# Kernel optimization log

Measured on AMD Instinct MI355X. Metric: run time of the kernel, lower is better.

## Reference

```python
import jax, jax.numpy as jnp
import numpy as np

N_NODES = 100000


def _gcn_conv(x, W, b, src, dst, deg_inv_sqrt):
    # linear transform first (PyG GCNConv order): [N, F] @ [F, H]
    h = x @ W
    # symmetric normalization per edge: deg^-1/2[src] * deg^-1/2[dst]
    norm = deg_inv_sqrt[src] * deg_inv_sqrt[dst]
    msg = h[src] * norm[:, None]  # [E, H]
    out = jax.ops.segment_sum(msg, dst, num_segments=N_NODES)
    return out + b


def setup_inputs() -> dict:
    key = jax.random.key(0)
    k1, k2, k3, k4 = jax.random.split(key, 4)
    F_IN, H = 512, 512
    E = 800000
    x = jax.random.normal(k1, (N_NODES, F_IN), dtype=jnp.float32)
    edge_index = jax.random.randint(k2, (2, E), 0, N_NODES, dtype=jnp.int64)
    W1 = jax.random.normal(k3, (F_IN, H), dtype=jnp.float32) * (1.0 / np.sqrt(F_IN))
    b1 = jnp.zeros((H,), dtype=jnp.float32)
    W2 = jax.random.normal(k4, (H, H), dtype=jnp.float32) * (1.0 / np.sqrt(H))
    b2 = jnp.zeros((H,), dtype=jnp.float32)
    return {"x": x, "edge_index": edge_index, "W1": W1, "b1": b1, "W2": W2, "b2": b2}


def reference(x, edge_index, W1, b1, W2, b2):
    # add self loops (PyG GCNConv default add_self_loops=True)
    loop = jnp.arange(N_NODES, dtype=edge_index.dtype)
    src = jnp.concatenate([edge_index[0], loop])
    dst = jnp.concatenate([edge_index[1], loop])
    # degree of destination nodes (including self loops)
    deg = jax.ops.segment_sum(jnp.ones_like(dst, dtype=x.dtype), dst, num_segments=N_NODES)
    deg_inv_sqrt = jnp.where(deg > 0, jax.lax.rsqrt(jnp.maximum(deg, 1.0)), 0.0)
    h = jax.nn.relu(_gcn_conv(x, W1, b1, src, dst, deg_inv_sqrt))
    # dropout is identity at inference (training=False)
    out = _gcn_conv(h, W2, b2, src, dst, deg_inv_sqrt)
    return out
```

## Files before the change

kernel.cpp:

```cpp
#include <hip/hip_runtime.h>

#define N_NODES 100000
#define E_EDGES 800000
#define E_TOT   900000
#define F 512

typedef __attribute__((ext_vector_type(8))) short short8;
typedef __attribute__((ext_vector_type(4))) float f32x4;
typedef unsigned int u32;

__device__ __forceinline__ float bfu(unsigned int u) {
    union { unsigned int i; float f; } c; c.i = u << 16; return c.f;
}
__device__ __forceinline__ unsigned short f2b(float f) {
    union { float f; unsigned int u; } c; c.f = f;
    return (unsigned short)((c.u + 0x7fffu + ((c.u >> 16) & 1u)) >> 16);
}
__device__ __forceinline__ float fbits(unsigned int u) {
    union { unsigned int i; float f; } c; c.i = u; return c.f;
}
__device__ __forceinline__ unsigned int bits(float f) {
    union { float f; unsigned int i; } c; c.f = f; return c.i;
}
__device__ __forceinline__ void gload_lds16(const void* g, void* l) {
    __builtin_amdgcn_global_load_lds(
        (const __attribute__((address_space(1))) u32*)g,
        (__attribute__((address_space(3))) u32*)l, 16, 0, 0);
}

__global__ void k_init(unsigned int* deg, unsigned int* counter) {
    int i = blockIdx.x * 256 + threadIdx.x;
    if (i < N_NODES) deg[i] = 1u;
    if (i == 0) *counter = 0u;
}

__global__ void k_hist(const int* __restrict__ ei, unsigned int* deg) {
    int e = blockIdx.x * 256 + threadIdx.x;
    if (e < E_EDGES) atomicAdd(&deg[ei[E_EDGES + e]], 1u);
}

__global__ void k_disalloc(const unsigned int* __restrict__ deg, unsigned int* counter,
                           float* __restrict__ dis,
                           int2* __restrict__ seg, unsigned int* __restrict__ cursor) {
    int i = blockIdx.x * 256 + threadIdx.x;
    if (i < N_NODES) {
        unsigned int d = deg[i];
        dis[i] = rsqrtf((float)d);
        unsigned int p = atomicAdd(counter, d);
        seg[i] = make_int2((int)p, (int)(p + d));
        cursor[i] = p;
    }
}

__global__ void k_scatter(const int* __restrict__ ei, const float* __restrict__ dis,
                          unsigned int* __restrict__ cursor,
                          uint2* __restrict__ ev) {
    int e = blockIdx.x * 256 + threadIdx.x;
    if (e < E_TOT) {
        int s, d;
        if (e < E_EDGES) { s = ei[e]; d = ei[E_EDGES + e]; }
        else             { s = e - E_EDGES; d = s; }
        unsigned int p = atomicAdd(&cursor[d], 1u);
        ev[p] = make_uint2((unsigned)s, bits(dis[s] * dis[d]));
    }
}

__global__ void k_cvtX(const float* __restrict__ xin, unsigned short* __restrict__ xb) {
    int i = blockIdx.x * 256 + threadIdx.x;
    const f32x4* p = (const f32x4*)xin + (size_t)i * 2;
    f32x4 a = __builtin_nontemporal_load(p);
    f32x4 b = __builtin_nontemporal_load(p + 1);
    uint4 o;
    o.x = (unsigned)f2b(a[0]) | ((unsigned)f2b(a[1]) << 16);
    o.y = (unsigned)f2b(a[2]) | ((unsigned)f2b(a[3]) << 16);
    o.z = (unsigned)f2b(b[0]) | ((unsigned)f2b(b[1]) << 16);
    o.w = (unsigned)f2b(b[2]) | ((unsigned)f2b(b[3]) << 16);
    *(uint4*)(xb + (size_t)i * 8) = o;
}

__global__ void k_cvtW(const float* __restrict__ W1, const float* __restrict__ W2,
                       unsigned short* __restrict__ W1t, unsigned short* __restrict__ W2t) {
    int t = blockIdx.x * 256 + threadIdx.x;
    int which = t >= F * F;
    int u = t - which * F * F;
    int n = u >> 9, k = u & 511;
    const float* W = which ? W2 : W1;
    unsigned short* Wt = which ? W2t : W1t;
    Wt[u] = f2b(W[k * F + n]);
}

__global__ __launch_bounds__(256)
void gemm_bt(const unsigned short* __restrict__ A, const unsigned short* __restrict__ Bt,
             const float* __restrict__ bias,
             unsigned short* __restrict__ outb, float* __restrict__ outf,
             int relu, int M) {
    __shared__ unsigned short lsa[2][128 * 32];
    __shared__ unsigned short lsb[2][128 * 32];
    int bx = blockIdx.x;
    int by = blockIdx.y;
    int t  = threadIdx.x;
    int lane = t & 63, w = t >> 6;
    int wr = w >> 1, wc = w & 1;

    f32x4 acc[4][4];
    #pragma unroll
    for (int m = 0; m < 4; ++m)
        #pragma unroll
        for (int n = 0; n < 4; ++n)
            acc[m][n] = (f32x4){0.f, 0.f, 0.f, 0.f};

    int rowBase = bx * 128;

    int ar[2], br[2], akc[2];
    #pragma unroll
    for (int i = 0; i < 2; ++i) {
        int idx = i * 256 + t;
        int r = idx >> 2;
        akc[i] = (idx & 3) * 8;
        int ga = rowBase + r; if (ga >= M) ga = M - 1;
        ar[i] = ga;
        br[i] = by * 128 + r;
    }

    auto STAGE = [&](int buf, int k0) {
        #pragma unroll
        for (int i = 0; i < 2; ++i) {
            int idx = i * 256 + t;
            gload_lds16(A + (size_t)ar[i] * F + k0 + akc[i], &lsa[buf][idx * 8]);
            gload_lds16(Bt + (size_t)br[i] * F + k0 + akc[i], &lsb[buf][idx * 8]);
        }
    };
    auto COMPUTE = [&](int buf) {
        int koff = (lane >> 4) * 8;
        int rsel = lane & 15;
        short8 af[4], bfr[4];
        #pragma unroll
        for (int m = 0; m < 4; ++m)
            af[m] = *(short8*)&lsa[buf][(wr * 64 + m * 16 + rsel) * 32 + koff];
        #pragma unroll
        for (int n = 0; n < 4; ++n)
            bfr[n] = *(short8*)&lsb[buf][(wc * 64 + n * 16 + rsel) * 32 + koff];
        #pragma unroll
        for (int m = 0; m < 4; ++m)
            #pragma unroll
            for (int n = 0; n < 4; ++n)
                acc[m][n] = __builtin_amdgcn_mfma_f32_16x16x32_bf16(af[m], bfr[n], acc[m][n], 0, 0, 0);
    };

    STAGE(0, 0);
    __syncthreads();
    #pragma unroll
    for (int kp = 0; kp < 8; ++kp) {
        STAGE(1, (2 * kp + 1) * 32);
        COMPUTE(0);
        __syncthreads();
        if (kp < 7) STAGE(0, (2 * kp + 2) * 32);
        COMPUTE(1);
        __syncthreads();
    }

    int rq = (lane >> 4) * 4, cq = lane & 15;
    #pragma unroll
    for (int m = 0; m < 4; ++m)
        #pragma unroll
        for (int n = 0; n < 4; ++n) {
            int colv = by * 128 + wc * 64 + n * 16 + cq;
            float bv = bias[colv];
            #pragma unroll
            for (int j = 0; j < 4; ++j) {
                int row = rowBase + wr * 64 + m * 16 + rq + j;
                if (row < M) {
                    float v = acc[m][n][j] + bv;
                    if (relu) v = fmaxf(v, 0.f);
                    if (outb) outb[(size_t)row * F + colv] = f2b(v);
                    else __builtin_nontemporal_store(v, outf + (size_t)row * F + colv);
                }
            }
        }
}

__global__ __launch_bounds__(256)
void k_agg(const unsigned short* __restrict__ hin, const int2* __restrict__ seg,
           const uint2* __restrict__ ev,
           unsigned short* __restrict__ outb) {
    int node = blockIdx.x * 4 + (threadIdx.x >> 6);
    int lane = threadIdx.x & 63;
    if (node >= N_NODES) return;
    int2 se = seg[node];
    int e0 = se.x, e1 = se.y;
    float acc[8] = {0, 0, 0, 0, 0, 0, 0, 0};
    const unsigned short* base = hin + lane * 8;

    int e = e0;
    for (; e + 3 < e1; e += 4) {
        uint2 p0 = ev[e], p1 = ev[e + 1], p2 = ev[e + 2], p3 = ev[e + 3];
        uint4 v0 = *(const uint4*)(base + ((size_t)p0.x << 9));
        uint4 v1 = *(const uint4*)(base + ((size_t)p1.x << 9));
        uint4 v2 = *(const uint4*)(base + ((size_t)p2.x << 9));
        uint4 v3 = *(const uint4*)(base + ((size_t)p3.x << 9));
        float w0 = fbits(p0.y), w1 = fbits(p1.y), w2 = fbits(p2.y), w3 = fbits(p3.y);
        acc[0] += w0 * bfu(v0.x & 0xffffu); acc[1] += w0 * bfu(v0.x >> 16);
        acc[2] += w0 * bfu(v0.y & 0xffffu); acc[3] += w0 * bfu(v0.y >> 16);
        acc[4] += w0 * bfu(v0.z & 0xffffu); acc[5] += w0 * bfu(v0.z >> 16);
        acc[6] += w0 * bfu(v0.w & 0xffffu); acc[7] += w0 * bfu(v0.w >> 16);
        acc[0] += w1 * bfu(v1.x & 0xffffu); acc[1] += w1 * bfu(v1.x >> 16);
        acc[2] += w1 * bfu(v1.y & 0xffffu); acc[3] += w1 * bfu(v1.y >> 16);
        acc[4] += w1 * bfu(v1.z & 0xffffu); acc[5] += w1 * bfu(v1.z >> 16);
        acc[6] += w1 * bfu(v1.w & 0xffffu); acc[7] += w1 * bfu(v1.w >> 16);
        acc[0] += w2 * bfu(v2.x & 0xffffu); acc[1] += w2 * bfu(v2.x >> 16);
        acc[2] += w2 * bfu(v2.y & 0xffffu); acc[3] += w2 * bfu(v2.y >> 16);
        acc[4] += w2 * bfu(v2.z & 0xffffu); acc[5] += w2 * bfu(v2.z >> 16);
        acc[6] += w2 * bfu(v2.w & 0xffffu); acc[7] += w2 * bfu(v2.w >> 16);
        acc[0] += w3 * bfu(v3.x & 0xffffu); acc[1] += w3 * bfu(v3.x >> 16);
        acc[2] += w3 * bfu(v3.y & 0xffffu); acc[3] += w3 * bfu(v3.y >> 16);
        acc[4] += w3 * bfu(v3.z & 0xffffu); acc[5] += w3 * bfu(v3.z >> 16);
        acc[6] += w3 * bfu(v3.w & 0xffffu); acc[7] += w3 * bfu(v3.w >> 16);
    }
    for (; e < e1; ++e) {
        uint2 p = ev[e];
        uint4 v = *(const uint4*)(base + ((size_t)p.x << 9));
        float wv = fbits(p.y);
        acc[0] += wv * bfu(v.x & 0xffffu); acc[1] += wv * bfu(v.x >> 16);
        acc[2] += wv * bfu(v.y & 0xffffu); acc[3] += wv * bfu(v.y >> 16);
        acc[4] += wv * bfu(v.z & 0xffffu); acc[5] += wv * bfu(v.z >> 16);
        acc[6] += wv * bfu(v.w & 0xffffu); acc[7] += wv * bfu(v.w >> 16);
    }

    uint4 o;
    o.x = (unsigned)f2b(acc[0]) | ((unsigned)f2b(acc[1]) << 16);
    o.y = (unsigned)f2b(acc[2]) | ((unsigned)f2b(acc[3]) << 16);
    o.z = (unsigned)f2b(acc[4]) | ((unsigned)f2b(acc[5]) << 16);
    o.w = (unsigned)f2b(acc[6]) | ((unsigned)f2b(acc[7]) << 16);
    *(uint4*)(outb + (size_t)node * F + lane * 8) = o;
}

extern "C" void kernel_launch(void* const* d_in, const int* in_sizes, int n_in,
                              void* d_out, int out_size, void* d_ws, size_t ws_size,
                              hipStream_t stream) {
    const float* x  = (const float*)d_in[0];
    const int*   ei = (const int*)d_in[1];
    const float* W1 = (const float*)d_in[2];
    const float* b1 = (const float*)d_in[3];
    const float* W2 = (const float*)d_in[4];
    const float* b2 = (const float*)d_in[5];
    float* out = (float*)d_out;

    char* ws = (char*)d_ws;
    size_t off = 0;
    auto alloc = [&](size_t bytes) -> void* {
        off = (off + 255) & ~(size_t)255;
        void* p = ws + off;
        off += bytes;
        return p;
    };

    unsigned short* tb  = (unsigned short*)alloc((size_t)N_NODES * F * 2);
    unsigned short* W1t = (unsigned short*)alloc((size_t)F * F * 2);
    unsigned short* W2t = (unsigned short*)alloc((size_t)F * F * 2);
    unsigned int*   deg = (unsigned int*)alloc((size_t)N_NODES * 4);
    float*          dis = (float*)alloc((size_t)N_NODES * 4);
    int2*           seg = (int2*)alloc((size_t)N_NODES * 8);
    unsigned int*   cur = (unsigned int*)alloc((size_t)N_NODES * 4);
    unsigned int*   cnt = (unsigned int*)alloc(256);
    uint2*          ev  = (uint2*)alloc((size_t)E_TOT * 8);

    unsigned short* h1b = (unsigned short*)d_out;
    unsigned short* xb  = (unsigned short*)((char*)d_out + (size_t)N_NODES * F * 2);

    int nb = (N_NODES + 255) / 256;

    k_init<<<nb, 256, 0, stream>>>(deg, cnt);
    k_hist<<<(E_EDGES + 255) / 256, 256, 0, stream>>>(ei, deg);
    k_disalloc<<<nb, 256, 0, stream>>>(deg, cnt, dis, seg, cur);
    k_scatter<<<(E_TOT + 255) / 256, 256, 0, stream>>>(ei, dis, cur, ev);

    k_cvtW<<<(2 * F * F) / 256, 256, 0, stream>>>(W1, W2, W1t, W2t);
    k_cvtX<<<(N_NODES * F / 8) / 256, 256, 0, stream>>>(x, xb);

    dim3 ggrid((N_NODES + 127) / 128, F / 128);

    k_agg<<<(N_NODES + 3) / 4, 256, 0, stream>>>(xb, seg, ev, tb);
    gemm_bt<<<ggrid, 256, 0, stream>>>(tb, W1t, b1, h1b, nullptr, 1, N_NODES);

    k_agg<<<(N_NODES + 3) / 4, 256, 0, stream>>>(h1b, seg, ev, tb);
    gemm_bt<<<ggrid, 256, 0, stream>>>(tb, W2t, b2, nullptr, out, 0, N_NODES);
}
```

Measured before the change: 685.2 us.

## Enlarge GEMM tiles to 256x256, remap blocks per XCD, stage bf16 output via LDS

The bf16 GEMM moves from 128x128 tiles with 256 threads to 256x256 tiles with 512 threads and a K-step of 64 per stage. Workgroup IDs are remapped so neighbouring tiles land on the same XCD, which should improve L2 reuse of the A rows. The bf16 output is written to LDS first and then stored to global memory as coalesced 16-byte writes. The aggregation loop is unrolled to 8 edges so more gather loads are in flight; the larger tiles use 128 KB of LDS and many accumulator registers, which can lower occupancy.

```diff
diff --git a/kernel.cpp b/kernel.cpp
--- a/kernel.cpp
+++ b/kernel.cpp
@@ -89,94 +89,133 @@
     Wt[u] = f2b(W[k * F + n]);
 }
 
-__global__ __launch_bounds__(256)
+__global__ __launch_bounds__(512, 2)
 void gemm_bt(const unsigned short* __restrict__ A, const unsigned short* __restrict__ Bt,
              const float* __restrict__ bias,
              unsigned short* __restrict__ outb, float* __restrict__ outf,
              int relu, int M) {
-    __shared__ unsigned short lsa[2][128 * 32];
-    __shared__ unsigned short lsb[2][128 * 32];
-    int bx = blockIdx.x;
-    int by = blockIdx.y;
+    __shared__ unsigned short sm[65536];
+
+    int nwg = gridDim.x * gridDim.y;
+    int orig = blockIdx.y * gridDim.x + blockIdx.x;
+    int q = nwg >> 3, r = nwg & 7;
+    int xcd = orig & 7, j8 = orig >> 3;
+    int wgid = (xcd < r ? xcd * (q + 1) : r * (q + 1) + (xcd - r) * q) + j8;
+    int by = wgid & 1;
+    int bx = wgid >> 1;
+
     int t  = threadIdx.x;
     int lane = t & 63, w = t >> 6;
-    int wr = w >> 1, wc = w & 1;
-
-    f32x4 acc[4][4];
+    int wr = w >> 2, wc = w & 3;
+    int rsel = lane & 15, khalf = (lane >> 4) * 8;
+
+    f32x4 acc[8][4];
     #pragma unroll
-    for (int m = 0; m < 4; ++m)
+    for (int m = 0; m < 8; ++m)
         #pragma unroll
         for (int n = 0; n < 4; ++n)
             acc[m][n] = (f32x4){0.f, 0.f, 0.f, 0.f};
 
-    int rowBase = bx * 128;
-
-    int ar[2], br[2], akc[2];
+    int rowBase = bx * 256;
+
+    int ar[4], br[4], kcc[4];
     #pragma unroll
-    for (int i = 0; i < 2; ++i) {
-        int idx = i * 256 + t;
-        int r = idx >> 2;
-        akc[i] = (idx & 3) * 8;
-        int ga = rowBase + r; if (ga >= M) ga = M - 1;
+    for (int i = 0; i < 4; ++i) {
+        int idx = i * 512 + t;
+        int rr = idx >> 3;
+        kcc[i] = (idx & 7) * 8;
+        int ga = rowBase + rr; if (ga >= M) ga = M - 1;
         ar[i] = ga;
-        br[i] = by * 128 + r;
+        br[i] = by * 256 + rr;
     }
 
     auto STAGE = [&](int buf, int k0) {
         #pragma unroll
-        for (int i = 0; i < 2; ++i) {
-            int idx = i * 256 + t;
-            gload_lds16(A + (size_t)ar[i] * F + k0 + akc[i], &lsa[buf][idx * 8]);
-            gload_lds16(Bt + (size_t)br[i] * F + k0 + akc[i], &lsb[buf][idx * 8]);
+        for (int i = 0; i < 4; ++i) {
+            int idx = i * 512 + t;
+            gload_lds16(A + (size_t)ar[i] * F + k0 + kcc[i], sm + buf * 16384 + idx * 8);
+            gload_lds16(Bt + (size_t)br[i] * F + k0 + kcc[i], sm + 32768 + buf * 16384 + idx * 8);
         }
     };
     auto COMPUTE = [&](int buf) {
-        int koff = (lane >> 4) * 8;
-        int rsel = lane & 15;
-        short8 af[4], bfr[4];
-        #pragma unroll
-        for (int m = 0; m < 4; ++m)
-            af[m] = *(short8*)&lsa[buf][(wr * 64 + m * 16 + rsel) * 32 + koff];
-        #pragma unroll
-        for (int n = 0; n < 4; ++n)
-            bfr[n] = *(short8*)&lsb[buf][(wc * 64 + n * 16 + rsel) * 32 + koff];
-        #pragma unroll
-        for (int m = 0; m < 4; ++m)
+        const unsigned short* la = sm + buf * 16384;
+        const unsigned short* lb = sm + 32768 + buf * 16384;
+        #pragma unroll
+        for (int ks = 0; ks < 2; ++ks) {
+            int koff = ks * 32 + khalf;
+            short8 af[8], bfr[4];
+            #pragma unroll
+            for (int m = 0; m < 8; ++m)
+                af[m] = *(const short8*)&la[(wr * 128 + m * 16 + rsel) * 64 + koff];
             #pragma unroll
             for (int n = 0; n < 4; ++n)
-                acc[m][n] = __builtin_amdgcn_mfma_f32_16x16x32_bf16(af[m], bfr[n], acc[m][n], 0, 0, 0);
+                bfr[n] = *(const short8*)&lb[(wc * 64 + n * 16 + rsel) * 64 + koff];
+            #pragma unroll
+            for (int m = 0; m < 8; ++m)
+                #pragma unroll
+                for (int n = 0; n < 4; ++n)
+                    acc[m][n] = __builtin_amdgcn_mfma_f32_16x16x32_bf16(af[m], bfr[n], acc[m][n], 0, 0, 0);
+        }
     };
 
     STAGE(0, 0);
     __syncthreads();
     #pragma unroll
-    for (int kp = 0; kp < 8; ++kp) {
-        STAGE(1, (2 * kp + 1) * 32);
+    for (int kp = 0; kp < 4; ++kp) {
+        STAGE(1, (2 * kp + 1) * 64);
         COMPUTE(0);
         __syncthreads();
-        if (kp < 7) STAGE(0, (2 * kp + 2) * 32);
+        if (kp < 3) STAGE(0, (2 * kp + 2) * 64);
         COMPUTE(1);
         __syncthreads();
     }
 
     int rq = (lane >> 4) * 4, cq = lane & 15;
-    #pragma unroll
-    for (int m = 0; m < 4; ++m)
-        #pragma unroll
-        for (int n = 0; n < 4; ++n) {
-            int colv = by * 128 + wc * 64 + n * 16 + cq;
-            float bv = bias[colv];
-            #pragma unroll
-            for (int j = 0; j < 4; ++j) {
-                int row = rowBase + wr * 64 + m * 16 + rq + j;
-                if (row < M) {
+    if (outb) {
+        #pragma unroll
+        for (int m = 0; m < 8; ++m)
+            #pragma unroll
+            for (int n = 0; n < 4; ++n) {
+                int cl = wc * 64 + n * 16 + cq;
+                float bv = bias[by * 256 + cl];
+                #pragma unroll
+                for (int j = 0; j < 4; ++j) {
+                    int rl = wr * 128 + m * 16 + rq + j;
                     float v = acc[m][n][j] + bv;
                     if (relu) v = fmaxf(v, 0.f);
-                    if (outb) outb[(size_t)row * F + colv] = f2b(v);
-                    else __builtin_nontemporal_store(v, outf + (size_t)row * F + colv);
+                    sm[rl * 256 + cl] = f2b(v);
                 }
             }
+        __syncthreads();
+        #pragma unroll
+        for (int p = 0; p < 16; ++p) {
+            int sidx = p * 4096 + t * 8;
+            int row = sidx >> 8;
+            int col = sidx & 255;
+            int grow = rowBase + row;
+            if (grow < M) {
+                uint4 v = *(const uint4*)&sm[sidx];
+                *(uint4*)&outb[(size_t)grow * F + by * 256 + col] = v;
+            }
         }
+    } else {
+        #pragma unroll
+        for (int m = 0; m < 8; ++m)
+            #pragma unroll
+            for (int n = 0; n < 4; ++n) {
+                int colv = by * 256 + wc * 64 + n * 16 + cq;
+                float bv = bias[colv];
+                #pragma unroll
+                for (int j = 0; j < 4; ++j) {
+                    int row = rowBase + wr * 128 + m * 16 + rq + j;
+                    if (row < M) {
+                        float v = acc[m][n][j] + bv;
+                        if (relu) v = fmaxf(v, 0.f);
+                        __builtin_nontemporal_store(v, outf + (size_t)row * F + colv);
+                    }
+                }
+            }
+    }
 }
 
 __global__ __launch_bounds__(256)
@@ -192,13 +231,20 @@
     const unsigned short* base = hin + lane * 8;
 
     int e = e0;
-    for (; e + 3 < e1; e += 4) {
-        uint2 p0 = ev[e], p1 = ev[e + 1], p2 = ev[e + 2], p3 = ev[e + 3];
+    int n8 = e0 + ((e1 - e0) & ~7);
+    for (; e < n8; e += 8) {
+        uint2 p0 = ev[e],     p1 = ev[e + 1], p2 = ev[e + 2], p3 = ev[e + 3];
+        uint2 p4 = ev[e + 4], p5 = ev[e + 5], p6 = ev[e + 6], p7 = ev[e + 7];
         uint4 v0 = *(const uint4*)(base + ((size_t)p0.x << 9));
         uint4 v1 = *(const uint4*)(base + ((size_t)p1.x << 9));
         uint4 v2 = *(const uint4*)(base + ((size_t)p2.x << 9));
         uint4 v3 = *(const uint4*)(base + ((size_t)p3.x << 9));
+        uint4 v4 = *(const uint4*)(base + ((size_t)p4.x << 9));
+        uint4 v5 = *(const uint4*)(base + ((size_t)p5.x << 9));
+        uint4 v6 = *(const uint4*)(base + ((size_t)p6.x << 9));
+        uint4 v7 = *(const uint4*)(base + ((size_t)p7.x << 9));
         float w0 = fbits(p0.y), w1 = fbits(p1.y), w2 = fbits(p2.y), w3 = fbits(p3.y);
+        float w4 = fbits(p4.y), w5 = fbits(p5.y), w6 = fbits(p6.y), w7 = fbits(p7.y);
         acc[0] += w0 * bfu(v0.x & 0xffffu); acc[1] += w0 * bfu(v0.x >> 16);
         acc[2] += w0 * bfu(v0.y & 0xffffu); acc[3] += w0 * bfu(v0.y >> 16);
         acc[4] += w0 * bfu(v0.z & 0xffffu); acc[5] += w0 * bfu(v0.z >> 16);
@@ -215,6 +261,22 @@
         acc[2] += w3 * bfu(v3.y & 0xffffu); acc[3] += w3 * bfu(v3.y >> 16);
         acc[4] += w3 * bfu(v3.z & 0xffffu); acc[5] += w3 * bfu(v3.z >> 16);
         acc[6] += w3 * bfu(v3.w & 0xffffu); acc[7] += w3 * bfu(v3.w >> 16);
+        acc[0] += w4 * bfu(v4.x & 0xffffu); acc[1] += w4 * bfu(v4.x >> 16);
+        acc[2] += w4 * bfu(v4.y & 0xffffu); acc[3] += w4 * bfu(v4.y >> 16);
+        acc[4] += w4 * bfu(v4.z & 0xffffu); acc[5] += w4 * bfu(v4.z >> 16);
+        acc[6] += w4 * bfu(v4.w & 0xffffu); acc[7] += w4 * bfu(v4.w >> 16);
+        acc[0] += w5 * bfu(v5.x & 0xffffu); acc[1] += w5 * bfu(v5.x >> 16);
+        acc[2] += w5 * bfu(v5.y & 0xffffu); acc[3] += w5 * bfu(v5.y >> 16);
+        acc[4] += w5 * bfu(v5.z & 0xffffu); acc[5] += w5 * bfu(v5.z >> 16);
+        acc[6] += w5 * bfu(v5.w & 0xffffu); acc[7] += w5 * bfu(v5.w >> 16);
+        acc[0] += w6 * bfu(v6.x & 0xffffu); acc[1] += w6 * bfu(v6.x >> 16);
+        acc[2] += w6 * bfu(v6.y & 0xffffu); acc[3] += w6 * bfu(v6.y >> 16);
+        acc[4] += w6 * bfu(v6.z & 0xffffu); acc[5] += w6 * bfu(v6.z >> 16);
+        acc[6] += w6 * bfu(v6.w & 0xffffu); acc[7] += w6 * bfu(v6.w >> 16);
+        acc[0] += w7 * bfu(v7.x & 0xffffu); acc[1] += w7 * bfu(v7.x >> 16);
+        acc[2] += w7 * bfu(v7.y & 0xffffu); acc[3] += w7 * bfu(v7.y >> 16);
+        acc[4] += w7 * bfu(v7.z & 0xffffu); acc[5] += w7 * bfu(v7.z >> 16);
+        acc[6] += w7 * bfu(v7.w & 0xffffu); acc[7] += w7 * bfu(v7.w >> 16);
     }
     for (; e < e1; ++e) {
         uint2 p = ev[e];
@@ -277,11 +339,11 @@
     k_cvtW<<<(2 * F * F) / 256, 256, 0, stream>>>(W1, W2, W1t, W2t);
     k_cvtX<<<(N_NODES * F / 8) / 256, 256, 0, stream>>>(x, xb);
 
-    dim3 ggrid((N_NODES + 127) / 128, F / 128);
+    dim3 ggrid(2, (N_NODES + 255) / 256);
 
     k_agg<<<(N_NODES + 3) / 4, 256, 0, stream>>>(xb, seg, ev, tb);
-    gemm_bt<<<ggrid, 256, 0, stream>>>(tb, W1t, b1, h1b, nullptr, 1, N_NODES);
+    gemm_bt<<<ggrid, 512, 0, stream>>>(tb, W1t, b1, h1b, nullptr, 1, N_NODES);
 
     k_agg<<<(N_NODES + 3) / 4, 256, 0, stream>>>(h1b, seg, ev, tb);
-    gemm_bt<<<ggrid, 256, 0, stream>>>(tb, W2t, b2, nullptr, out, 0, N_NODES);
-}
+    gemm_bt<<<ggrid, 512, 0, stream>>>(tb, W2t, b2, nullptr, out, 0, N_NODES);
+}
```

Result: faster. 647.3 us (-5.5%).
